# Performance work log

Measured on AMD Instinct MI355X. Metric: run time of the kernel, lower is better.

Reference implementation:

```python
import jax, jax.numpy as jnp
import numpy as np

DT = 0.1
K = 262144


def _skew(v):
    # v: [k,3] -> [k,3,3]
    x, y, z = v[..., 0], v[..., 1], v[..., 2]
    O = jnp.zeros_like(x)
    return jnp.stack([
        jnp.stack([O, -z, y], -1),
        jnp.stack([z, O, -x], -1),
        jnp.stack([-y, x, O], -1)], -2)


def _se3_exp(t):
    # t: [k,6] twist = [rho(linear), phi(angular)] -> (R [k,3,3], p [k,3])
    rho, phi = t[:, :3], t[:, 3:]
    th2 = jnp.sum(phi * phi, -1)
    small = th2 < 1e-8
    th2s = jnp.where(small, 1.0, th2)        # safe denominator
    th = jnp.sqrt(th2s)
    A = jnp.where(small, 1.0 - th2 / 6.0, jnp.sin(th) / th)
    B = jnp.where(small, 0.5 - th2 / 24.0, (1.0 - jnp.cos(th)) / th2s)
    C = jnp.where(small, 1.0 / 6.0 - th2 / 120.0, (th - jnp.sin(th)) / (th2s * th))
    S = _skew(phi)
    S2 = S @ S
    I = jnp.eye(3, dtype=t.dtype)
    R = I + A[:, None, None] * S + B[:, None, None] * S2
    V = I + B[:, None, None] * S + C[:, None, None] * S2
    p = jnp.einsum('kij,kj->ki', V, rho)
    return R, p


def _adjoint(R, p):
    # SE3 adjoint for twist order [linear, angular]: [[R, [p]x R],[0, R]]
    top = jnp.concatenate([R, _skew(p) @ R], -1)
    bot = jnp.concatenate([jnp.zeros_like(R), R], -1)
    return jnp.concatenate([top, bot], -2)  # [k,6,6]


def setup_inputs() -> dict:
    key = jax.random.key(0)
    ks = jax.random.split(key, 8)
    s = jax.random.normal(ks[0], (K, 1, 18), dtype=jnp.float32) * 0.1
    # state layout: [pos(3), rot(9), twist(6)]; rotation must be a valid R (identity, as in fake_state)
    s = s.at[:, :, 3:12].set(jnp.eye(3, dtype=jnp.float32).reshape(9))
    a = jax.random.normal(ks[1], (K, 1, 6), dtype=jnp.float32) * 0.1
    h0 = jnp.zeros((1, K, 12), dtype=jnp.float32)
    W_ih = jax.random.normal(ks[2], (12, 21), dtype=jnp.float32) / np.sqrt(21)
    W_hh = jax.random.normal(ks[3], (12, 12), dtype=jnp.float32) / np.sqrt(12)
    W1 = jax.random.normal(ks[4], (128, 12), dtype=jnp.float32) / np.sqrt(12)
    W2 = jax.random.normal(ks[5], (128, 128), dtype=jnp.float32) / np.sqrt(128)
    W3 = jax.random.normal(ks[6], (6, 128), dtype=jnp.float32) / np.sqrt(128)
    return {"s": s, "a": a, "h0": h0, "W_ih": W_ih, "W_hh": W_hh, "W1": W1, "W2": W2, "W3": W3}


def reference(s, a, h0, W_ih, W_hh, W1, W2, W3):
    k = s.shape[0]
    # RNN input: pose-rot+vel (cols 3:) concat action -> [k, 21] (tau=1)
    x = jnp.concatenate([s[:, :, 3:], a], -1)[:, 0]
    h1 = jnp.tanh(x @ W_ih.T + h0[0] @ W_hh.T)          # [k,12] single RNN step, no bias
    hN = h1[None]                                        # [1,k,12]
    lrelu = lambda z: jnp.where(z >= 0, z, 0.1 * z)
    dv = lrelu(lrelu(h1 @ W1.T) @ W2.T) @ W3.T           # [k,6]
    v = s[:, -1, -6:]                                    # body twist
    p = s[:, -1, :3]
    R = s[:, -1, 3:12].reshape(k, 3, 3)
    # SE3 integration: M_next = M_current @ Exp(v*dt)
    Re, pe = _se3_exp(v * DT)
    R_next = R @ Re
    p_next = jnp.einsum('kij,kj->ki', R, pe) + p
    # M_next^-1
    Rinv = jnp.swapaxes(R_next, -1, -2)
    pinv = -jnp.einsum('kij,kj->ki', Rinv, p_next)
    # velocity update through adjoints
    vI = jnp.einsum('kij,kj->ki', _adjoint(R, p), v)
    v_next = jnp.einsum('kij,kj->ki', _adjoint(Rinv, pinv), vI + dv)
    s_next = jnp.concatenate([p_next, R_next.reshape(k, 9), v_next], -1)[:, None, :]
    return s_next, hN, dv
```

## Files before the change

### kernel.cpp

```cpp
#include <hip/hip_runtime.h>
#include <math.h>

typedef __attribute__((ext_vector_type(8))) short short8;
typedef __attribute__((ext_vector_type(4))) float f32x4;

#define DT_STEP 0.1f

static __device__ __forceinline__ unsigned bf16rne(float f) {
    unsigned u = __builtin_bit_cast(unsigned, f);
    return (u + 0x7fffu + ((u >> 16) & 1u)) >> 16;
}
static __device__ __forceinline__ unsigned bf16pk2(float lo, float hi) {
    unsigned r;
    asm("v_cvt_pk_bf16_f32 %0, %1, %2" : "=v"(r) : "v"(lo), "v"(hi));
    return r;
}
static __device__ __forceinline__ float tanh_fast(float v) {
    float e = __expf(2.0f * v);
    return 1.0f - 2.0f / (e + 1.0f);
}

static __device__ __forceinline__ uint4 tr_read8(unsigned a) {
    uint2 lo, hi;
    asm volatile("ds_read_b64_tr_b16 %0, %2 offset:0\n\t"
                 "ds_read_b64_tr_b16 %1, %2 offset:128"
                 : "=&v"(lo), "=&v"(hi) : "v"(a));
    return make_uint4(lo.x, lo.y, hi.x, hi.y);
}

static __device__ __forceinline__ void mm3(const float* A, const float* B, float* C) {
#pragma unroll
    for (int i = 0; i < 3; ++i)
#pragma unroll
        for (int j = 0; j < 3; ++j)
            C[i * 3 + j] = A[i * 3 + 0] * B[0 * 3 + j] + A[i * 3 + 1] * B[1 * 3 + j] + A[i * 3 + 2] * B[2 * 3 + j];
}
static __device__ __forceinline__ void mv3(const float* A, const float* x, float* y) {
#pragma unroll
    for (int i = 0; i < 3; ++i) y[i] = A[i * 3 + 0] * x[0] + A[i * 3 + 1] * x[1] + A[i * 3 + 2] * x[2];
}
static __device__ __forceinline__ void mtv3(const float* A, const float* x, float* y) {
#pragma unroll
    for (int i = 0; i < 3; ++i) y[i] = A[0 * 3 + i] * x[0] + A[1 * 3 + i] * x[1] + A[2 * 3 + i] * x[2];
}
static __device__ __forceinline__ void cross3(const float* p, const float* u, float* y) {
    y[0] = p[1] * u[2] - p[2] * u[1];
    y[1] = p[2] * u[0] - p[0] * u[2];
    y[2] = p[0] * u[1] - p[1] * u[0];
}

__global__ __launch_bounds__(256)
void weights_prep(const float* __restrict__ W1, const float* __restrict__ W2,
                  const float* __restrict__ W3, unsigned short* __restrict__ ws) {
    int i = blockIdx.x * 256 + threadIdx.x;
    if (i < 4096) {
        int n = i >> 5, k = i & 31;
        ws[i] = (k < 12) ? (unsigned short)bf16rne(W1[n * 12 + k]) : (unsigned short)0;
    } else if (i < 20480) {
        ws[i] = (unsigned short)bf16rne(W2[i - 4096]);
    } else if (i < 22528) {
        int j = i - 20480;
        int jj = j & 7;
        int l = (j >> 3) & 15;
        int kl = j >> 7;
        int k = kl * 8 + jj;
        ws[i] = (l < 6) ? (unsigned short)bf16rne(W3[l * 128 + k]) : (unsigned short)0;
    }
}

__global__ __launch_bounds__(256, 2)
void auv_mfma6_kernel(const float* __restrict__ s, const float* __restrict__ a,
                      const float* __restrict__ h0, const float* __restrict__ W_ih,
                      const float* __restrict__ W_hh, const unsigned short* __restrict__ Wbf,
                      float* __restrict__ out, int K)
{
    __shared__ __align__(16) char lds[4][18432];
    const int tid  = threadIdx.x;
    const int wid  = tid >> 6;
    const int lane = tid & 63;
    const int l15  = lane & 15;
    const int lg   = lane >> 4;

    char* base = &lds[wid][0];
    char* h1t  = base;
    char* l12  = base + 2048;
    char* dvt  = h1t;

    const unsigned lds_off = (unsigned)(size_t)l12;
    const unsigned trb     = lds_off + lg * 256 + l15 * 8;
    const unsigned stoff   = ((l15 >> 2) << 7) + ((l15 & 3) << 5) + (lg << 3);

    const unsigned short* W1A = Wbf;
    const unsigned short* W2B = Wbf + 4096;
    const unsigned short* W3B = Wbf + 20480;

    const int e_raw = blockIdx.x * 256 + wid * 64 + lane;
    const int e  = e_raw < K ? e_raw : K - 1;
    const bool live = e_raw < K;

    const float* srow = s  + (size_t)e * 18;
    const float* arow = a  + (size_t)e * 6;
    const float* hrow = h0 + (size_t)e * 12;

    float xv[21];
#pragma unroll
    for (int i = 0; i < 15; ++i) xv[i] = srow[3 + i];
#pragma unroll
    for (int i = 0; i < 6; ++i)  xv[15 + i] = arow[i];
    float h0v[12];
#pragma unroll
    for (int i = 0; i < 12; ++i) h0v[i] = hrow[i];

    float h1v[12];
#pragma unroll
    for (int j = 0; j < 12; ++j) {
        float acc = 0.f;
        const float* wih = W_ih + j * 21;
#pragma unroll
        for (int i = 0; i < 21; ++i) acc = fmaf(wih[i], xv[i], acc);
        const float* whh = W_hh + j * 12;
#pragma unroll
        for (int i = 0; i < 12; ++i) acc = fmaf(whh[i], h0v[i], acc);
        h1v[j] = tanh_fast(acc);
    }

    if (live) {
        float4* h4 = (float4*)(out + (size_t)K * 18 + (size_t)e * 12);
        h4[0] = make_float4(h1v[0], h1v[1], h1v[2], h1v[3]);
        h4[1] = make_float4(h1v[4], h1v[5], h1v[6], h1v[7]);
        h4[2] = make_float4(h1v[8], h1v[9], h1v[10], h1v[11]);
    }

    {
        unsigned p0 = bf16pk2(h1v[0], h1v[1]);
        unsigned p1 = bf16pk2(h1v[2], h1v[3]);
        unsigned p2 = bf16pk2(h1v[4], h1v[5]);
        unsigned p3 = bf16pk2(h1v[6], h1v[7]);
        unsigned p4 = bf16pk2(h1v[8], h1v[9]);
        unsigned p5 = bf16pk2(h1v[10], h1v[11]);
        int rq = (lane & 1) << 4;
        *(uint4*)(h1t + lane * 32 + (0 ^ rq))  = make_uint4(p0, p1, p2, p3);
        *(uint4*)(h1t + lane * 32 + (16 ^ rq)) = make_uint4(p4, p5, 0u, 0u);
    }
    asm volatile("s_waitcnt lgkmcnt(0)" ::: "memory");
    __builtin_amdgcn_sched_barrier(0);

    const short8 zfrag = {0, 0, 0, 0, 0, 0, 0, 0};

    short8 af1[4];
#pragma unroll
    for (int rt = 0; rt < 4; ++rt) {
        af1[rt] = zfrag;
        if (lg < 2) {
            int row = rt * 16 + l15;
            af1[rt] = __builtin_bit_cast(short8,
                *(const uint4*)(h1t + row * 32 + ((lg * 16) ^ ((row & 1) << 4))));
        }
    }
#pragma unroll 1
    for (int nt = 0; nt < 8; ++nt) {
        short8 b1 = __builtin_bit_cast(short8,
            *(const uint4*)(W1A + ((nt * 16 + l15) * 32 + lg * 8)));
#pragma unroll
        for (int rt = 0; rt < 4; ++rt) {
            f32x4 z = {0.f, 0.f, 0.f, 0.f};
            f32x4 c1 = __builtin_amdgcn_mfma_f32_16x16x32_bf16(af1[rt], b1, z, 0, 0, 0);
            float v0 = fmaxf(c1[0], 0.1f * c1[0]);
            float v1 = fmaxf(c1[1], 0.1f * c1[1]);
            float v2 = fmaxf(c1[2], 0.1f * c1[2]);
            float v3 = fmaxf(c1[3], 0.1f * c1[3]);
            *(uint2*)(l12 + rt * 4096 + nt * 512 + stoff) =
                make_uint2(bf16pk2(v0, v1), bf16pk2(v2, v3));
        }
    }
    asm volatile("s_waitcnt lgkmcnt(0)" ::: "memory");
    __builtin_amdgcn_sched_barrier(0);

    short8 af2[4][4];
#pragma unroll
    for (int rt = 0; rt < 4; ++rt)
#pragma unroll
        for (int kt = 0; kt < 4; ++kt)
            af2[rt][kt] = __builtin_bit_cast(short8, tr_read8(trb + rt * 4096 + kt * 1024));
    asm volatile("s_waitcnt lgkmcnt(0)" ::: "memory");
    __builtin_amdgcn_sched_barrier(0);

    short8 bfr[4];
#pragma unroll
    for (int kt = 0; kt < 4; ++kt)
        bfr[kt] = __builtin_bit_cast(short8,
            *(const uint4*)(W2B + (l15 * 128 + kt * 32 + lg * 8)));

#pragma unroll 1
    for (int nt = 0; nt < 8; ++nt) {
        short8 bnext[4];
        if (nt < 7) {
#pragma unroll
            for (int kt = 0; kt < 4; ++kt)
                bnext[kt] = __builtin_bit_cast(short8,
                    *(const uint4*)(W2B + (((nt + 1) * 16 + l15) * 128 + kt * 32 + lg * 8)));
        }
#pragma unroll
        for (int rt = 0; rt < 4; ++rt) {
            f32x4 c2 = {0.f, 0.f, 0.f, 0.f};
#pragma unroll
            for (int kt = 0; kt < 4; ++kt)
                c2 = __builtin_amdgcn_mfma_f32_16x16x32_bf16(af2[rt][kt], bfr[kt], c2, 0, 0, 0);
            float v0 = fmaxf(c2[0], 0.1f * c2[0]);
            float v1 = fmaxf(c2[1], 0.1f * c2[1]);
            float v2 = fmaxf(c2[2], 0.1f * c2[2]);
            float v3 = fmaxf(c2[3], 0.1f * c2[3]);
            *(uint2*)(l12 + rt * 4096 + nt * 512 + stoff) =
                make_uint2(bf16pk2(v0, v1), bf16pk2(v2, v3));
        }
#pragma unroll
        for (int kt = 0; kt < 4; ++kt) bfr[kt] = bnext[kt];
    }
    asm volatile("s_waitcnt lgkmcnt(0)" ::: "memory");
    __builtin_amdgcn_sched_barrier(0);

    short8 af3[4][4];
#pragma unroll
    for (int rt = 0; rt < 4; ++rt)
#pragma unroll
        for (int kt = 0; kt < 4; ++kt)
            af3[rt][kt] = __builtin_bit_cast(short8, tr_read8(trb + rt * 4096 + kt * 1024));
    asm volatile("s_waitcnt lgkmcnt(0)" ::: "memory");
    __builtin_amdgcn_sched_barrier(0);

    f32x4 c3[4];
#pragma unroll
    for (int rt = 0; rt < 4; ++rt) c3[rt] = (f32x4){0.f, 0.f, 0.f, 0.f};
#pragma unroll
    for (int kt = 0; kt < 4; ++kt) {
        short8 b3 = __builtin_bit_cast(short8,
            *(const uint4*)(W3B + (((kt * 4 + lg) * 16 + l15) * 8)));
#pragma unroll
        for (int rt = 0; rt < 4; ++rt)
            c3[rt] = __builtin_amdgcn_mfma_f32_16x16x32_bf16(af3[rt][kt], b3, c3[rt], 0, 0, 0);
    }

    float dvv[6];
    if (l15 < 6) {
#pragma unroll
        for (int rt = 0; rt < 4; ++rt)
#pragma unroll
            for (int r = 0; r < 4; ++r) {
                int row = rt * 16 + lg * 4 + r;
                *(float*)(dvt + row * 32 + l15 * 4) = c3[rt][r];
            }
    }
    asm volatile("s_waitcnt lgkmcnt(0)" ::: "memory");
    __builtin_amdgcn_sched_barrier(0);
    {
        const float* dr = (const float*)(dvt + lane * 32);
        dvv[0] = dr[0]; dvv[1] = dr[1]; dvv[2] = dr[2];
        dvv[3] = dr[3]; dvv[4] = dr[4]; dvv[5] = dr[5];
    }
    asm volatile("s_waitcnt lgkmcnt(0)" ::: "memory");
    __builtin_amdgcn_sched_barrier(0);

    float sv[18];
#pragma unroll
    for (int i = 0; i < 18; ++i) sv[i] = srow[i];
    const float* v = &sv[12];
    const float* p = &sv[0];
    const float* R = &sv[3];

    float rho[3] = {v[0] * DT_STEP, v[1] * DT_STEP, v[2] * DT_STEP};
    float phi[3] = {v[3] * DT_STEP, v[4] * DT_STEP, v[5] * DT_STEP};
    float th2 = phi[0] * phi[0] + phi[1] * phi[1] + phi[2] * phi[2];

    float A, B, C;
    if (th2 < 1e-8f) {
        A = 1.0f - th2 * (1.0f / 6.0f);
        B = 0.5f - th2 * (1.0f / 24.0f);
        C = (1.0f / 6.0f) - th2 * (1.0f / 120.0f);
    } else {
        float th = sqrtf(th2);
        float sn = sinf(th), cs = cosf(th);
        A = sn / th;
        B = (1.0f - cs) / th2;
        C = (th - sn) / (th2 * th);
    }

    float S[9] = {0.f, -phi[2], phi[1], phi[2], 0.f, -phi[0], -phi[1], phi[0], 0.f};
    float S2[9];
    mm3(S, S, S2);

    float Re[9], V[9];
#pragma unroll
    for (int i = 0; i < 9; ++i) {
        float I = (i == 0 || i == 4 || i == 8) ? 1.0f : 0.0f;
        Re[i] = I + A * S[i] + B * S2[i];
        V[i]  = I + B * S[i] + C * S2[i];
    }

    float pe[3];
    mv3(V, rho, pe);
    float Rn[9];
    mm3(R, Re, Rn);
    float pn[3];
    mv3(R, pe, pn);
    pn[0] += p[0]; pn[1] += p[1]; pn[2] += p[2];

    float pinv[3];
    mtv3(Rn, pn, pinv);
    pinv[0] = -pinv[0]; pinv[1] = -pinv[1]; pinv[2] = -pinv[2];

    float Rvl[3], Rva[3];
    mv3(R, &v[0], Rvl);
    mv3(R, &v[3], Rva);
    float px[3];
    cross3(p, Rva, px);
    float u6[6];
    u6[0] = Rvl[0] + px[0] + dvv[0];
    u6[1] = Rvl[1] + px[1] + dvv[1];
    u6[2] = Rvl[2] + px[2] + dvv[2];
    u6[3] = Rva[0] + dvv[3];
    u6[4] = Rva[1] + dvv[4];
    u6[5] = Rva[2] + dvv[5];

    float Rul[3], Rua[3];
    mtv3(Rn, &u6[0], Rul);
    mtv3(Rn, &u6[3], Rua);
    float pxu[3];
    cross3(pinv, Rua, pxu);
    float vn[6];
    vn[0] = Rul[0] + pxu[0];
    vn[1] = Rul[1] + pxu[1];
    vn[2] = Rul[2] + pxu[2];
    vn[3] = Rua[0];
    vn[4] = Rua[1];
    vn[5] = Rua[2];

    if (live) {
        float* s_next = out + (size_t)e * 18;
        s_next[0] = pn[0]; s_next[1] = pn[1]; s_next[2] = pn[2];
#pragma unroll
        for (int i = 0; i < 9; ++i) s_next[3 + i] = Rn[i];
#pragma unroll
        for (int i = 0; i < 6; ++i) s_next[12 + i] = vn[i];

        float* dvo = out + (size_t)K * 30 + (size_t)e * 6;
#pragma unroll
        for (int r = 0; r < 6; ++r) dvo[r] = dvv[r];
    }
}

extern "C" void kernel_launch(void* const* d_in, const int* in_sizes, int n_in,
                              void* d_out, int out_size, void* d_ws, size_t ws_size,
                              hipStream_t stream) {
    const float* s    = (const float*)d_in[0];
    const float* a    = (const float*)d_in[1];
    const float* h0   = (const float*)d_in[2];
    const float* W_ih = (const float*)d_in[3];
    const float* W_hh = (const float*)d_in[4];
    const float* W1   = (const float*)d_in[5];
    const float* W2   = (const float*)d_in[6];
    const float* W3   = (const float*)d_in[7];

    int K = in_sizes[0] / 18;
    unsigned short* ws = (unsigned short*)d_ws;

    weights_prep<<<(22528 + 255) / 256, 256, 0, stream>>>(W1, W2, W3, ws);

    int grid = (K + 255) / 256;
    auv_mfma6_kernel<<<grid, 256, 0, stream>>>(s, a, h0, W_ih, W_hh, ws,
                                               (float*)d_out, K);
}
```

Baseline: 55.80 us.

## Use single-wave blocks and overlap SE3 math with MLP LDS traffic

Switches from 256-thread blocks with four per-wave LDS slices to 64-thread blocks with a 16KB LDS buffer each, and raises the launch-bounds occupancy hint. It also hoists the W2 and W3 fragment loads and the SE3 pose-integration math ahead of the final LDS waits, so global loads and ALU work overlap with the MFMA layers. Register pressure goes up because the SE3 intermediates stay live across the third GEMM, and the grid becomes four times larger.

```diff
diff --git a/kernel.cpp b/kernel.cpp
--- a/kernel.cpp
+++ b/kernel.cpp
@@ -68,33 +68,29 @@
     }
 }
 
-__global__ __launch_bounds__(256, 2)
-void auv_mfma6_kernel(const float* __restrict__ s, const float* __restrict__ a,
+__global__ __launch_bounds__(64, 3)
+void auv_mfma7_kernel(const float* __restrict__ s, const float* __restrict__ a,
                       const float* __restrict__ h0, const float* __restrict__ W_ih,
                       const float* __restrict__ W_hh, const unsigned short* __restrict__ Wbf,
                       float* __restrict__ out, int K)
 {
-    __shared__ __align__(16) char lds[4][18432];
-    const int tid  = threadIdx.x;
-    const int wid  = tid >> 6;
-    const int lane = tid & 63;
+    __shared__ __align__(16) char lds[16384];
+    const int lane = threadIdx.x & 63;
     const int l15  = lane & 15;
     const int lg   = lane >> 4;
 
-    char* base = &lds[wid][0];
-    char* h1t  = base;
-    char* l12  = base + 2048;
-    char* dvt  = h1t;
-
-    const unsigned lds_off = (unsigned)(size_t)l12;
-    const unsigned trb     = lds_off + lg * 256 + l15 * 8;
-    const unsigned stoff   = ((l15 >> 2) << 7) + ((l15 & 3) << 5) + (lg << 3);
+    char* l12 = &lds[0];
+    char* h1t = &lds[0];
+    char* dvt = &lds[0];
+
+    const unsigned trb   = (unsigned)(lg * 256 + l15 * 8);
+    const unsigned stoff = ((l15 >> 2) << 7) + ((l15 & 3) << 5) + (lg << 3);
 
     const unsigned short* W1A = Wbf;
     const unsigned short* W2B = Wbf + 4096;
     const unsigned short* W3B = Wbf + 20480;
 
-    const int e_raw = blockIdx.x * 256 + wid * 64 + lane;
+    const int e_raw = blockIdx.x * 64 + lane;
     const int e  = e_raw < K ? e_raw : K - 1;
     const bool live = e_raw < K;
 
@@ -130,6 +126,12 @@
         h4[1] = make_float4(h1v[4], h1v[5], h1v[6], h1v[7]);
         h4[2] = make_float4(h1v[8], h1v[9], h1v[10], h1v[11]);
     }
+
+    short8 bfr[4];
+#pragma unroll
+    for (int kt = 0; kt < 4; ++kt)
+        bfr[kt] = __builtin_bit_cast(short8,
+            *(const uint4*)(W2B + (l15 * 128 + kt * 32 + lg * 8)));
 
     {
         unsigned p0 = bf16pk2(h1v[0], h1v[1]);
@@ -157,6 +159,9 @@
                 *(const uint4*)(h1t + row * 32 + ((lg * 16) ^ ((row & 1) << 4))));
         }
     }
+    asm volatile("s_waitcnt lgkmcnt(0)" ::: "memory");
+    __builtin_amdgcn_sched_barrier(0);
+
 #pragma unroll 1
     for (int nt = 0; nt < 8; ++nt) {
         short8 b1 = __builtin_bit_cast(short8,
@@ -185,12 +190,6 @@
     asm volatile("s_waitcnt lgkmcnt(0)" ::: "memory");
     __builtin_amdgcn_sched_barrier(0);
 
-    short8 bfr[4];
-#pragma unroll
-    for (int kt = 0; kt < 4; ++kt)
-        bfr[kt] = __builtin_bit_cast(short8,
-            *(const uint4*)(W2B + (l15 * 128 + kt * 32 + lg * 8)));
-
 #pragma unroll 1
     for (int nt = 0; nt < 8; ++nt) {
         short8 bnext[4];
@@ -225,6 +224,65 @@
 #pragma unroll
         for (int kt = 0; kt < 4; ++kt)
             af3[rt][kt] = __builtin_bit_cast(short8, tr_read8(trb + rt * 4096 + kt * 1024));
+
+    short8 b3f[4];
+#pragma unroll
+    for (int kt = 0; kt < 4; ++kt)
+        b3f[kt] = __builtin_bit_cast(short8,
+            *(const uint4*)(W3B + (((kt * 4 + lg) * 16 + l15) * 8)));
+
+    float sv[18];
+#pragma unroll
+    for (int i = 0; i < 18; ++i) sv[i] = srow[i];
+    const float* v = &sv[12];
+    const float* p = &sv[0];
+    const float* R = &sv[3];
+
+    float Rn[9], pn[3], pinv[3], Rvl[3], Rva[3], px[3];
+    {
+        float rho[3] = {v[0] * DT_STEP, v[1] * DT_STEP, v[2] * DT_STEP};
+        float phi[3] = {v[3] * DT_STEP, v[4] * DT_STEP, v[5] * DT_STEP};
+        float th2 = phi[0] * phi[0] + phi[1] * phi[1] + phi[2] * phi[2];
+
+        float A, B, C;
+        if (th2 < 1e-8f) {
+            A = 1.0f - th2 * (1.0f / 6.0f);
+            B = 0.5f - th2 * (1.0f / 24.0f);
+            C = (1.0f / 6.0f) - th2 * (1.0f / 120.0f);
+        } else {
+            float th = sqrtf(th2);
+            float sn = sinf(th), cs = cosf(th);
+            A = sn / th;
+            B = (1.0f - cs) / th2;
+            C = (th - sn) / (th2 * th);
+        }
+
+        float S[9] = {0.f, -phi[2], phi[1], phi[2], 0.f, -phi[0], -phi[1], phi[0], 0.f};
+        float S2[9];
+        mm3(S, S, S2);
+
+        float Re[9], V[9];
+#pragma unroll
+        for (int i = 0; i < 9; ++i) {
+            float I = (i == 0 || i == 4 || i == 8) ? 1.0f : 0.0f;
+            Re[i] = I + A * S[i] + B * S2[i];
+            V[i]  = I + B * S[i] + C * S2[i];
+        }
+
+        float pe[3];
+        mv3(V, rho, pe);
+        mm3(R, Re, Rn);
+        mv3(R, pe, pn);
+        pn[0] += p[0]; pn[1] += p[1]; pn[2] += p[2];
+
+        mtv3(Rn, pn, pinv);
+        pinv[0] = -pinv[0]; pinv[1] = -pinv[1]; pinv[2] = -pinv[2];
+
+        mv3(R, &v[0], Rvl);
+        mv3(R, &v[3], Rva);
+        cross3(p, Rva, px);
+    }
+
     asm volatile("s_waitcnt lgkmcnt(0)" ::: "memory");
     __builtin_amdgcn_sched_barrier(0);
 
@@ -233,11 +291,9 @@
     for (int rt = 0; rt < 4; ++rt) c3[rt] = (f32x4){0.f, 0.f, 0.f, 0.f};
 #pragma unroll
     for (int kt = 0; kt < 4; ++kt) {
-        short8 b3 = __builtin_bit_cast(short8,
-            *(const uint4*)(W3B + (((kt * 4 + lg) * 16 + l15) * 8)));
 #pragma unroll
         for (int rt = 0; rt < 4; ++rt)
-            c3[rt] = __builtin_amdgcn_mfma_f32_16x16x32_bf16(af3[rt][kt], b3, c3[rt], 0, 0, 0);
+            c3[rt] = __builtin_amdgcn_mfma_f32_16x16x32_bf16(af3[rt][kt], b3f[kt], c3[rt], 0, 0, 0);
     }
 
     float dvv[6];
@@ -257,62 +313,7 @@
         dvv[0] = dr[0]; dvv[1] = dr[1]; dvv[2] = dr[2];
         dvv[3] = dr[3]; dvv[4] = dr[4]; dvv[5] = dr[5];
     }
-    asm volatile("s_waitcnt lgkmcnt(0)" ::: "memory");
-    __builtin_amdgcn_sched_barrier(0);
-
-    float sv[18];
-#pragma unroll
-    for (int i = 0; i < 18; ++i) sv[i] = srow[i];
-    const float* v = &sv[12];
-    const float* p = &sv[0];
-    const float* R = &sv[3];
-
-    float rho[3] = {v[0] * DT_STEP, v[1] * DT_STEP, v[2] * DT_STEP};
-    float phi[3] = {v[3] * DT_STEP, v[4] * DT_STEP, v[5] * DT_STEP};
-    float th2 = phi[0] * phi[0] + phi[1] * phi[1] + phi[2] * phi[2];
-
-    float A, B, C;
-    if (th2 < 1e-8f) {
-        A = 1.0f - th2 * (1.0f / 6.0f);
-        B = 0.5f - th2 * (1.0f / 24.0f);
-        C = (1.0f / 6.0f) - th2 * (1.0f / 120.0f);
-    } else {
-        float th = sqrtf(th2);
-        float sn = sinf(th), cs = cosf(th);
-        A = sn / th;
-        B = (1.0f - cs) / th2;
-        C = (th - sn) / (th2 * th);
-    }
-
-    float S[9] = {0.f, -phi[2], phi[1], phi[2], 0.f, -phi[0], -phi[1], phi[0], 0.f};
-    float S2[9];
-    mm3(S, S, S2);
-
-    float Re[9], V[9];
-#pragma unroll
-    for (int i = 0; i < 9; ++i) {
-        float I = (i == 0 || i == 4 || i == 8) ? 1.0f : 0.0f;
-        Re[i] = I + A * S[i] + B * S2[i];
-        V[i]  = I + B * S[i] + C * S2[i];
-    }
-
-    float pe[3];
-    mv3(V, rho, pe);
-    float Rn[9];
-    mm3(R, Re, Rn);
-    float pn[3];
-    mv3(R, pe, pn);
-    pn[0] += p[0]; pn[1] += p[1]; pn[2] += p[2];
-
-    float pinv[3];
-    mtv3(Rn, pn, pinv);
-    pinv[0] = -pinv[0]; pinv[1] = -pinv[1]; pinv[2] = -pinv[2];
-
-    float Rvl[3], Rva[3];
-    mv3(R, &v[0], Rvl);
-    mv3(R, &v[3], Rva);
-    float px[3];
-    cross3(p, Rva, px);
+
     float u6[6];
     u6[0] = Rvl[0] + px[0] + dvv[0];
     u6[1] = Rvl[1] + px[1] + dvv[1];
@@ -365,7 +366,7 @@
 
     weights_prep<<<(22528 + 255) / 256, 256, 0, stream>>>(W1, W2, W3, ws);
 
-    int grid = (K + 255) / 256;
-    auv_mfma6_kernel<<<grid, 256, 0, stream>>>(s, a, h0, W_ih, W_hh, ws,
-                                               (float*)d_out, K);
-}
+    int grid = (K + 63) / 64;
+    auv_mfma7_kernel<<<grid, 64, 0, stream>>>(s, a, h0, W_ih, W_hh, ws,
+                                              (float*)d_out, K);
+}
```

After: 53.20 us. -4.7%, faster.
